# Performance work log

Hardware: AMD Instinct MI355X
Metric: run time of the kernel (lower is better)

## Reference

```python
import jax, jax.numpy as jnp
import numpy as np

N_NODES = 100000
N_EDGES = 1600000
IN_FEATS = 64
OUT_FEATS = 64
DIM = 3
N_KERNELS = 4


def setup_inputs() -> dict:
    key = jax.random.key(0)
    ks = jax.random.split(key, 8)
    feat = jax.random.normal(ks[0], (N_NODES, IN_FEATS), dtype=jnp.float32)
    pseudo = jax.random.uniform(ks[1], (N_EDGES, DIM), dtype=jnp.float32)
    src = jax.random.randint(ks[2], (N_EDGES,), 0, N_NODES, dtype=jnp.int32)
    dst = jax.random.randint(ks[3], (N_EDGES,), 0, N_NODES, dtype=jnp.int32)
    W_fc = jax.random.normal(ks[4], (N_KERNELS * OUT_FEATS, IN_FEATS), dtype=jnp.float32) * 0.1
    mu = jax.random.normal(ks[5], (N_KERNELS, DIM), dtype=jnp.float32)
    inv_sigma = jax.random.uniform(ks[6], (N_KERNELS, DIM), dtype=jnp.float32) + 0.5
    bias = jnp.zeros((OUT_FEATS,), dtype=jnp.float32)
    return {"feat": feat, "pseudo": pseudo, "src": src, "dst": dst,
            "W_fc": W_fc, "mu": mu, "inv_sigma": inv_sigma, "bias": bias}


def reference(feat, pseudo, src, dst, W_fc, mu, inv_sigma, bias):
    N = feat.shape[0]
    K, out = N_KERNELS, OUT_FEATS
    # node projections: [N, K, out]
    h = (feat @ W_fc.T).reshape(N, K, out)
    # per-edge Gaussian kernel weights: [E, K]
    diff = pseudo[:, None, :] - mu[None, :, :]            # [E, K, dim]
    g = jnp.exp(jnp.sum(-0.5 * diff * diff * (inv_sigma[None] ** 2), axis=-1))
    # sum-aggregate: sum_k sum_{e: dst=v} h[src_e, k] * g[e, k]
    # (kernel sum and edge sum commute for sum reducer; loop over K avoids [E,K,out])
    rst = jnp.zeros((N, out), dtype=feat.dtype)
    for k in range(K):
        msg = h[:, k, :][src] * g[:, k:k + 1]             # [E, out]
        rst = rst + jax.ops.segment_sum(msg, dst, num_segments=N)
    # residual (Identity since in_feats == out_feats) + bias
    rst = rst + feat + bias
    return rst
```

## Files before the change

kernel.cpp:

```cpp
#include <hip/hip_runtime.h>

#define N_NODES_C 100000
#define N_EDGES_C 1600000
#define IN_F 64
#define OUT_F 64
#define NK 4
#define SCAN_BLK 256
#define NBLK ((N_NODES_C + SCAN_BLK - 1) / SCAN_BLK)
#define EBLK (N_EDGES_C / 256)
#define CPAD 16
#define NSLICE 8
#define SLICE_N (N_NODES_C / NSLICE)
#define SCAT_GRID 2048

__device__ __forceinline__ unsigned int f2bf(float x) {
    unsigned int u = __float_as_uint(x);
    return (u + 0x7fffu + ((u >> 16) & 1u)) >> 16;
}
__device__ __forceinline__ float bflo(unsigned int u) { return __uint_as_float(u << 16); }
__device__ __forceinline__ float bfhi(unsigned int u) { return __uint_as_float(u & 0xffff0000u); }

__global__ __launch_bounds__(256) void hist_kernel(
    const int* __restrict__ dst, int* __restrict__ cnt)
{
    const int slice = (int)blockIdx.x & 7;
    const int w     = (int)blockIdx.x >> 3;
    const int lo = slice * SLICE_N, hi = lo + SLICE_N;
    for (int c = w; c < EBLK; c += SCAT_GRID / NSLICE) {
        const int d = dst[c * 256 + (int)threadIdx.x];
        if (d >= lo && d < hi) atomicAdd(&cnt[d], 1);
    }
}

__global__ __launch_bounds__(256, 2) void proj_kernel(
    const float* __restrict__ feat, const float* __restrict__ W,
    unsigned short* __restrict__ hb, int n_nodes)
{
    __shared__ float frow[4][IN_F];
    const int t = threadIdx.x;
    const int o = t >> 2;
    const int k = t & 3;
    float wreg[IN_F];
    {
        const float4* W4 = reinterpret_cast<const float4*>(W + (size_t)(k * OUT_F + o) * IN_F);
        #pragma unroll
        for (int i = 0; i < IN_F / 4; ++i) {
            float4 v = W4[i];
            wreg[4*i+0] = v.x; wreg[4*i+1] = v.y; wreg[4*i+2] = v.z; wreg[4*i+3] = v.w;
        }
    }
    const int nn4 = n_nodes >> 2;
    for (int q = blockIdx.x; q < nn4; q += gridDim.x) {
        const int n0 = q << 2;
        if (t < 64) {
            float4 v = reinterpret_cast<const float4*>(feat + (size_t)n0 * IN_F)[t];
            reinterpret_cast<float4*>(frow[t >> 4])[t & 15] = v;
        }
        __syncthreads();
        const float4* f0 = reinterpret_cast<const float4*>(frow[0]);
        const float4* f1 = reinterpret_cast<const float4*>(frow[1]);
        const float4* f2 = reinterpret_cast<const float4*>(frow[2]);
        const float4* f3 = reinterpret_cast<const float4*>(frow[3]);
        float a0 = 0.f, a1 = 0.f, a2 = 0.f, a3 = 0.f;
        #pragma unroll
        for (int i = 0; i < IN_F / 4; ++i) {
            const float4 v0 = f0[i], v1 = f1[i], v2 = f2[i], v3 = f3[i];
            const float w0 = wreg[4*i], w1 = wreg[4*i+1], w2 = wreg[4*i+2], w3 = wreg[4*i+3];
            a0 = fmaf(v0.x,w0, fmaf(v0.y,w1, fmaf(v0.z,w2, fmaf(v0.w,w3, a0))));
            a1 = fmaf(v1.x,w0, fmaf(v1.y,w1, fmaf(v1.z,w2, fmaf(v1.w,w3, a1))));
            a2 = fmaf(v2.x,w0, fmaf(v2.y,w1, fmaf(v2.z,w2, fmaf(v2.w,w3, a2))));
            a3 = fmaf(v3.x,w0, fmaf(v3.y,w1, fmaf(v3.z,w2, fmaf(v3.w,w3, a3))));
        }
        hb[(size_t)(n0+0) * 256 + t] = (unsigned short)f2bf(a0);
        hb[(size_t)(n0+1) * 256 + t] = (unsigned short)f2bf(a1);
        hb[(size_t)(n0+2) * 256 + t] = (unsigned short)f2bf(a2);
        hb[(size_t)(n0+3) * 256 + t] = (unsigned short)f2bf(a3);
        __syncthreads();
    }
}

__global__ __launch_bounds__(256) void scan1_kernel(
    const int* __restrict__ cnt, int* __restrict__ bsum)
{
    __shared__ int s[SCAN_BLK];
    int i = blockIdx.x * SCAN_BLK + threadIdx.x;
    int v = (i < N_NODES_C) ? cnt[i] : 0;
    s[threadIdx.x] = v; __syncthreads();
    for (int off = SCAN_BLK / 2; off > 0; off >>= 1) {
        if (threadIdx.x < off) s[threadIdx.x] += s[threadIdx.x + off];
        __syncthreads();
    }
    if (threadIdx.x == 0) bsum[blockIdx.x] = s[0];
}

__global__ __launch_bounds__(256) void scan23_kernel(
    const int* __restrict__ cnt, const int* __restrict__ bsum,
    int* __restrict__ row_start, int* __restrict__ cursor_pad)
{
    __shared__ int pre[SCAN_BLK];
    __shared__ int s[SCAN_BLK];
    const int t = threadIdx.x;
    int p = 0;
    for (int i = t; i < (int)blockIdx.x; i += SCAN_BLK) p += bsum[i];
    pre[t] = p; __syncthreads();
    for (int off = SCAN_BLK / 2; off > 0; off >>= 1) {
        if (t < off) pre[t] += pre[t + off];
        __syncthreads();
    }
    const int boff = pre[0];
    const int i = blockIdx.x * SCAN_BLK + t;
    int v = (i < N_NODES_C) ? cnt[i] : 0;
    s[t] = v; __syncthreads();
    for (int off = 1; off < SCAN_BLK; off <<= 1) {
        int x = (t >= off) ? s[t - off] : 0;
        __syncthreads();
        s[t] += x;
        __syncthreads();
    }
    if (i < N_NODES_C) {
        int ex = s[t] - v + boff;
        row_start[i] = ex;
        cursor_pad[(size_t)i * CPAD] = ex;
        if (i == N_NODES_C - 1) row_start[N_NODES_C] = ex + v;
    }
}

__global__ __launch_bounds__(256) void scatter_kernel(
    const int* __restrict__ src, const int* __restrict__ dst,
    const float* __restrict__ pseudo, const float* __restrict__ mu,
    const float* __restrict__ inv_sigma, int* __restrict__ cursor_pad,
    uint4* __restrict__ rec)
{
    float mm[NK*3], ss[NK*3];
    #pragma unroll
    for (int i = 0; i < NK*3; ++i) { mm[i] = mu[i]; ss[i] = inv_sigma[i]; }
    const int slice = (int)blockIdx.x & 7;
    const int w     = (int)blockIdx.x >> 3;
    const int lo = slice * SLICE_N, hi = lo + SLICE_N;
    for (int c = w; c < EBLK; c += SCAT_GRID / NSLICE) {
        const int e = c * 256 + (int)threadIdx.x;
        const int d = dst[e];
        if (d >= lo && d < hi) {
            const float p0 = pseudo[(size_t)e * 3 + 0];
            const float p1 = pseudo[(size_t)e * 3 + 1];
            const float p2 = pseudo[(size_t)e * 3 + 2];
            float g[NK];
            #pragma unroll
            for (int k = 0; k < NK; ++k) {
                const float d0 = p0 - mm[k*3+0], d1 = p1 - mm[k*3+1], d2 = p2 - mm[k*3+2];
                const float s0 = ss[k*3+0], s1 = ss[k*3+1], s2 = ss[k*3+2];
                g[k] = __expf(-0.5f * (d0*d0*s0*s0 + d1*d1*s1*s1 + d2*d2*s2*s2));
            }
            const int pos = atomicAdd(&cursor_pad[(size_t)d * CPAD], 1);
            uint4 r;
            r.x = (unsigned int)src[e];
            r.y = f2bf(g[0]) | (f2bf(g[1]) << 16);
            r.z = f2bf(g[2]) | (f2bf(g[3]) << 16);
            r.w = 0u;
            rec[pos] = r;
        }
    }
}

__global__ __launch_bounds__(256, 2) void gather_kernel(
    const int* __restrict__ row_start, const uint4* __restrict__ rec,
    const unsigned short* __restrict__ hb,
    const float* __restrict__ feat, const float* __restrict__ bias,
    float* __restrict__ out, int n_nodes)
{
    const int lane = threadIdx.x & 63;
    const int v = (blockIdx.x * 256 + threadIdx.x) >> 6;
    if (v >= n_nodes) return;
    const int r0 = row_start[v];
    const int r1 = row_start[v + 1];
    float acc = 0.f;
    int j = r0;
    const int jend4 = r0 + ((r1 - r0) & ~3);
    if (j < jend4) {
        uint4 a0 = rec[j+0], a1 = rec[j+1], a2 = rec[j+2], a3 = rec[j+3];
        j += 4;
        for (; j < jend4; j += 4) {
            const uint2 h0 = *(const uint2*)(hb + (size_t)a0.x * 256 + lane * 4);
            const uint2 h1 = *(const uint2*)(hb + (size_t)a1.x * 256 + lane * 4);
            const uint2 h2 = *(const uint2*)(hb + (size_t)a2.x * 256 + lane * 4);
            const uint2 h3 = *(const uint2*)(hb + (size_t)a3.x * 256 + lane * 4);
            const uint4 b0 = rec[j+0], b1 = rec[j+1], b2 = rec[j+2], b3 = rec[j+3];
            acc += bflo(a0.y)*bflo(h0.x) + bfhi(a0.y)*bfhi(h0.x)
                 + bflo(a0.z)*bflo(h0.y) + bfhi(a0.z)*bfhi(h0.y);
            acc += bflo(a1.y)*bflo(h1.x) + bfhi(a1.y)*bfhi(h1.x)
                 + bflo(a1.z)*bflo(h1.y) + bfhi(a1.z)*bfhi(h1.y);
            acc += bflo(a2.y)*bflo(h2.x) + bfhi(a2.y)*bfhi(h2.x)
                 + bflo(a2.z)*bflo(h2.y) + bfhi(a2.z)*bfhi(h2.y);
            acc += bflo(a3.y)*bflo(h3.x) + bfhi(a3.y)*bfhi(h3.x)
                 + bflo(a3.z)*bflo(h3.y) + bfhi(a3.z)*bfhi(h3.y);
            a0 = b0; a1 = b1; a2 = b2; a3 = b3;
        }
        {
            const uint2 h0 = *(const uint2*)(hb + (size_t)a0.x * 256 + lane * 4);
            const uint2 h1 = *(const uint2*)(hb + (size_t)a1.x * 256 + lane * 4);
            const uint2 h2 = *(const uint2*)(hb + (size_t)a2.x * 256 + lane * 4);
            const uint2 h3 = *(const uint2*)(hb + (size_t)a3.x * 256 + lane * 4);
            acc += bflo(a0.y)*bflo(h0.x) + bfhi(a0.y)*bfhi(h0.x)
                 + bflo(a0.z)*bflo(h0.y) + bfhi(a0.z)*bfhi(h0.y);
            acc += bflo(a1.y)*bflo(h1.x) + bfhi(a1.y)*bfhi(h1.x)
                 + bflo(a1.z)*bflo(h1.y) + bfhi(a1.z)*bfhi(h1.y);
            acc += bflo(a2.y)*bflo(h2.x) + bfhi(a2.y)*bfhi(h2.x)
                 + bflo(a2.z)*bflo(h2.y) + bfhi(a2.z)*bfhi(h2.y);
            acc += bflo(a3.y)*bflo(h3.x) + bfhi(a3.y)*bfhi(h3.x)
                 + bflo(a3.z)*bflo(h3.y) + bfhi(a3.z)*bfhi(h3.y);
        }
    }
    for (; j < r1; ++j) {
        const uint4 ra = rec[j];
        const uint2 ha = *(const uint2*)(hb + (size_t)ra.x * 256 + lane * 4);
        acc += bflo(ra.y)*bflo(ha.x) + bfhi(ra.y)*bfhi(ha.x)
             + bflo(ra.z)*bflo(ha.y) + bfhi(ra.z)*bfhi(ha.y);
    }
    out[(size_t)v * OUT_F + lane] = acc + feat[(size_t)v * OUT_F + lane] + bias[lane];
}

extern "C" void kernel_launch(void* const* d_in, const int* in_sizes, int n_in,
                              void* d_out, int out_size, void* d_ws, size_t ws_size,
                              hipStream_t stream) {
    const float* feat      = (const float*)d_in[0];
    const float* pseudo    = (const float*)d_in[1];
    const int*   src       = (const int*)d_in[2];
    const int*   dst       = (const int*)d_in[3];
    const float* W_fc      = (const float*)d_in[4];
    const float* mu        = (const float*)d_in[5];
    const float* inv_sigma = (const float*)d_in[6];
    const float* bias      = (const float*)d_in[7];
    float* out = (float*)d_out;

    char* ws = (char*)d_ws;
    unsigned short* hb = (unsigned short*)ws;  ws += (size_t)N_NODES_C * 256 * 2;
    uint4* rec         = (uint4*)ws;           ws += (size_t)N_EDGES_C * 16;
    int* cursor_pad    = (int*)ws;             ws += (size_t)N_NODES_C * CPAD * 4;
    int* cnt           = (int*)ws;             ws += (size_t)N_NODES_C * 4;
    int* row_start     = (int*)ws;             ws += (size_t)(N_NODES_C + 4) * 4;
    int* bsum          = (int*)ws;             ws += 512 * 4;

    hipMemsetAsync(cnt, 0, (size_t)N_NODES_C * 4, stream);
    hist_kernel<<<SCAT_GRID, 256, 0, stream>>>(dst, cnt);
    proj_kernel<<<2048, 256, 0, stream>>>(feat, W_fc, hb, N_NODES_C);
    scan1_kernel<<<NBLK, SCAN_BLK, 0, stream>>>(cnt, bsum);
    scan23_kernel<<<NBLK, SCAN_BLK, 0, stream>>>(cnt, bsum, row_start, cursor_pad);
    scatter_kernel<<<SCAT_GRID, 256, 0, stream>>>(src, dst, pseudo, mu, inv_sigma,
                                                  cursor_pad, rec);
    gather_kernel<<<(N_NODES_C * 64 + 255) / 256, 256, 0, stream>>>(
        row_start, rec, hb, feat, bias, out, N_NODES_C);
}
```

Baseline: 345.7 us.

## Pre-bin edges by destination slice instead of rescanning all edges per slice

Adds a two-pass binning stage (per-block slice counts, per-slice scan, stable placement) that writes (edge, dst) pairs into eight slice buckets. The histogram and scatter kernels then read only their own slice's bucket instead of every slice re-reading the full dst array and discarding most entries. This removes the eightfold redundant dst reads, but adds three kernel launches, a serial per-slice scan over 6250 entries, an extra intermediate buffer, and indirect loads of pseudo and src. It also assumes each slice bucket holds at most BCAP edges, which holds for uniform random dst but is a fixed capacity.

```diff
diff --git a/kernel.cpp b/kernel.cpp
--- a/kernel.cpp
+++ b/kernel.cpp
@@ -11,7 +11,9 @@
 #define CPAD 16
 #define NSLICE 8
 #define SLICE_N (N_NODES_C / NSLICE)
-#define SCAT_GRID 2048
+#define BCAP 204800
+#define SLICE_GRID 2048
+#define SLICE_W 65536
 
 __device__ __forceinline__ unsigned int f2bf(float x) {
     unsigned int u = __float_as_uint(x);
@@ -20,16 +22,70 @@
 __device__ __forceinline__ float bflo(unsigned int u) { return __uint_as_float(u << 16); }
 __device__ __forceinline__ float bfhi(unsigned int u) { return __uint_as_float(u & 0xffff0000u); }
 
+__global__ __launch_bounds__(256) void binA_kernel(
+    const int* __restrict__ dst, int* __restrict__ cnt8)
+{
+    __shared__ int lcnt[NSLICE];
+    const int t = threadIdx.x;
+    if (t < NSLICE) lcnt[t] = 0;
+    __syncthreads();
+    const int s8 = dst[blockIdx.x * 256 + t] / SLICE_N;
+    atomicAdd(&lcnt[s8], 1);
+    __syncthreads();
+    if (t < NSLICE) cnt8[blockIdx.x * NSLICE + t] = lcnt[t];
+}
+
+__global__ __launch_bounds__(256) void binscan_kernel(
+    int* __restrict__ cnt8, int* __restrict__ totals)
+{
+    __shared__ int sh[256];
+    const int s = blockIdx.x;
+    const int t = threadIdx.x;
+    int running = 0;
+    for (int c = 0; c < (EBLK + 255) / 256; ++c) {
+        const int idx = c * 256 + t;
+        int v = (idx < EBLK) ? cnt8[idx * NSLICE + s] : 0;
+        sh[t] = v; __syncthreads();
+        for (int off = 1; off < 256; off <<= 1) {
+            int x = (t >= off) ? sh[t - off] : 0;
+            __syncthreads();
+            sh[t] += x;
+            __syncthreads();
+        }
+        if (idx < EBLK) cnt8[idx * NSLICE + s] = sh[t] - v + running;
+        running += sh[255];
+        __syncthreads();
+    }
+    if (t == 0) totals[s] = running;
+}
+
+__global__ __launch_bounds__(256) void binB_kernel(
+    const int* __restrict__ dst, const int* __restrict__ cnt8,
+    uint2* __restrict__ binbuf)
+{
+    __shared__ int lcnt[NSLICE];
+    const int t = threadIdx.x;
+    if (t < NSLICE) lcnt[t] = 0;
+    __syncthreads();
+    const int e = blockIdx.x * 256 + t;
+    const int d = dst[e];
+    const int s8 = d / SLICE_N;
+    const int rank = atomicAdd(&lcnt[s8], 1);
+    const int pos = cnt8[blockIdx.x * NSLICE + s8] + rank;
+    uint2 r; r.x = (unsigned int)e; r.y = (unsigned int)d;
+    binbuf[(size_t)s8 * BCAP + pos] = r;
+}
+
 __global__ __launch_bounds__(256) void hist_kernel(
-    const int* __restrict__ dst, int* __restrict__ cnt)
+    const uint2* __restrict__ binbuf, const int* __restrict__ totals,
+    int* __restrict__ cnt)
 {
     const int slice = (int)blockIdx.x & 7;
-    const int w     = (int)blockIdx.x >> 3;
-    const int lo = slice * SLICE_N, hi = lo + SLICE_N;
-    for (int c = w; c < EBLK; c += SCAT_GRID / NSLICE) {
-        const int d = dst[c * 256 + (int)threadIdx.x];
-        if (d >= lo && d < hi) atomicAdd(&cnt[d], 1);
-    }
+    const int wid = (((int)blockIdx.x >> 3) << 8) + (int)threadIdx.x;
+    const int n = totals[slice];
+    const uint2* bin = binbuf + (size_t)slice * BCAP;
+    for (int i = wid; i < n; i += SLICE_W)
+        atomicAdd(&cnt[bin[i].y], 1);
 }
 
 __global__ __launch_bounds__(256, 2) void proj_kernel(
@@ -126,39 +182,39 @@
 }
 
 __global__ __launch_bounds__(256) void scatter_kernel(
-    const int* __restrict__ src, const int* __restrict__ dst,
-    const float* __restrict__ pseudo, const float* __restrict__ mu,
-    const float* __restrict__ inv_sigma, int* __restrict__ cursor_pad,
-    uint4* __restrict__ rec)
+    const uint2* __restrict__ binbuf, const int* __restrict__ totals,
+    const int* __restrict__ src, const float* __restrict__ pseudo,
+    const float* __restrict__ mu, const float* __restrict__ inv_sigma,
+    int* __restrict__ cursor_pad, uint4* __restrict__ rec)
 {
     float mm[NK*3], ss[NK*3];
     #pragma unroll
     for (int i = 0; i < NK*3; ++i) { mm[i] = mu[i]; ss[i] = inv_sigma[i]; }
     const int slice = (int)blockIdx.x & 7;
-    const int w     = (int)blockIdx.x >> 3;
-    const int lo = slice * SLICE_N, hi = lo + SLICE_N;
-    for (int c = w; c < EBLK; c += SCAT_GRID / NSLICE) {
-        const int e = c * 256 + (int)threadIdx.x;
-        const int d = dst[e];
-        if (d >= lo && d < hi) {
-            const float p0 = pseudo[(size_t)e * 3 + 0];
-            const float p1 = pseudo[(size_t)e * 3 + 1];
-            const float p2 = pseudo[(size_t)e * 3 + 2];
-            float g[NK];
-            #pragma unroll
-            for (int k = 0; k < NK; ++k) {
-                const float d0 = p0 - mm[k*3+0], d1 = p1 - mm[k*3+1], d2 = p2 - mm[k*3+2];
-                const float s0 = ss[k*3+0], s1 = ss[k*3+1], s2 = ss[k*3+2];
-                g[k] = __expf(-0.5f * (d0*d0*s0*s0 + d1*d1*s1*s1 + d2*d2*s2*s2));
-            }
-            const int pos = atomicAdd(&cursor_pad[(size_t)d * CPAD], 1);
-            uint4 r;
-            r.x = (unsigned int)src[e];
-            r.y = f2bf(g[0]) | (f2bf(g[1]) << 16);
-            r.z = f2bf(g[2]) | (f2bf(g[3]) << 16);
-            r.w = 0u;
-            rec[pos] = r;
-        }
+    const int wid = (((int)blockIdx.x >> 3) << 8) + (int)threadIdx.x;
+    const int n = totals[slice];
+    const uint2* bin = binbuf + (size_t)slice * BCAP;
+    for (int i = wid; i < n; i += SLICE_W) {
+        const uint2 ed = bin[i];
+        const int e = (int)ed.x;
+        const int d = (int)ed.y;
+        const float p0 = pseudo[(size_t)e * 3 + 0];
+        const float p1 = pseudo[(size_t)e * 3 + 1];
+        const float p2 = pseudo[(size_t)e * 3 + 2];
+        float g[NK];
+        #pragma unroll
+        for (int k = 0; k < NK; ++k) {
+            const float d0 = p0 - mm[k*3+0], d1 = p1 - mm[k*3+1], d2 = p2 - mm[k*3+2];
+            const float s0 = ss[k*3+0], s1 = ss[k*3+1], s2 = ss[k*3+2];
+            g[k] = __expf(-0.5f * (d0*d0*s0*s0 + d1*d1*s1*s1 + d2*d2*s2*s2));
+        }
+        const int pos = atomicAdd(&cursor_pad[(size_t)d * CPAD], 1);
+        uint4 r;
+        r.x = (unsigned int)src[e];
+        r.y = f2bf(g[0]) | (f2bf(g[1]) << 16);
+        r.z = f2bf(g[2]) | (f2bf(g[3]) << 16);
+        r.w = 0u;
+        rec[pos] = r;
     }
 }
 
@@ -235,18 +291,24 @@
     char* ws = (char*)d_ws;
     unsigned short* hb = (unsigned short*)ws;  ws += (size_t)N_NODES_C * 256 * 2;
     uint4* rec         = (uint4*)ws;           ws += (size_t)N_EDGES_C * 16;
+    uint2* binbuf      = (uint2*)ws;           ws += (size_t)NSLICE * BCAP * 8;
     int* cursor_pad    = (int*)ws;             ws += (size_t)N_NODES_C * CPAD * 4;
     int* cnt           = (int*)ws;             ws += (size_t)N_NODES_C * 4;
     int* row_start     = (int*)ws;             ws += (size_t)(N_NODES_C + 4) * 4;
+    int* cnt8          = (int*)ws;             ws += (size_t)EBLK * NSLICE * 4;
     int* bsum          = (int*)ws;             ws += 512 * 4;
+    int* totals        = (int*)ws;             ws += 64 * 4;
 
     hipMemsetAsync(cnt, 0, (size_t)N_NODES_C * 4, stream);
-    hist_kernel<<<SCAT_GRID, 256, 0, stream>>>(dst, cnt);
+    binA_kernel<<<EBLK, 256, 0, stream>>>(dst, cnt8);
+    binscan_kernel<<<NSLICE, 256, 0, stream>>>(cnt8, totals);
+    binB_kernel<<<EBLK, 256, 0, stream>>>(dst, cnt8, binbuf);
+    hist_kernel<<<SLICE_GRID, 256, 0, stream>>>(binbuf, totals, cnt);
     proj_kernel<<<2048, 256, 0, stream>>>(feat, W_fc, hb, N_NODES_C);
     scan1_kernel<<<NBLK, SCAN_BLK, 0, stream>>>(cnt, bsum);
     scan23_kernel<<<NBLK, SCAN_BLK, 0, stream>>>(cnt, bsum, row_start, cursor_pad);
-    scatter_kernel<<<SCAT_GRID, 256, 0, stream>>>(src, dst, pseudo, mu, inv_sigma,
-                                                  cursor_pad, rec);
+    scatter_kernel<<<SLICE_GRID, 256, 0, stream>>>(binbuf, totals, src, pseudo,
+                                                   mu, inv_sigma, cursor_pad, rec);
     gather_kernel<<<(N_NODES_C * 64 + 255) / 256, 256, 0, stream>>>(
         row_start, rec, hb, feat, bias, out, N_NODES_C);
 }
```

Result: slower. 385.3 us (+11.5%).
